# Optimization experiments

Hardware: AMD Instinct MI355X
Metric: run time of the kernel (lower is better)

## Reference

```python
import jax, jax.numpy as jnp
import numpy as np

N = 10000      # num_nodes
E = 320000     # num_edges (before self loops)
F_IN = 256     # num_features
H = 128        # hidden_channels
C = 2          # num_classes
NEG_SLOPE = 0.2  # PyG GATConv default leaky_relu slope


def setup_inputs() -> dict:
    key = jax.random.key(0)
    ks = jax.random.split(key, 12)
    x = jax.random.normal(ks[0], (N, F_IN), dtype=jnp.float32)
    edge_index = jax.random.randint(ks[1], (2, E), 0, N, dtype=jnp.int32)
    s = 0.05
    return {
        "x": x,
        "edge_index": edge_index,
        # GATConv layer 1 (heads=1): lin (no bias), att_src, att_dst, bias
        "W1": jax.random.normal(ks[2], (F_IN, H), dtype=jnp.float32) * s,
        "att_src1": jax.random.normal(ks[3], (H,), dtype=jnp.float32) * s,
        "att_dst1": jax.random.normal(ks[4], (H,), dtype=jnp.float32) * s,
        "b1": jnp.zeros((H,), dtype=jnp.float32),
        # GATConv layer 2
        "W2": jax.random.normal(ks[5], (H, H), dtype=jnp.float32) * s,
        "att_src2": jax.random.normal(ks[6], (H,), dtype=jnp.float32) * s,
        "att_dst2": jax.random.normal(ks[7], (H,), dtype=jnp.float32) * s,
        "b2": jnp.zeros((H,), dtype=jnp.float32),
        # reduce_dim: Linear(H, 1)
        "Wr": jax.random.normal(ks[8], (H, 1), dtype=jnp.float32) * s,
        "br": jnp.zeros((1,), dtype=jnp.float32),
        # classifier: Linear(N, C)
        "Wc": jax.random.normal(ks[9], (N, C), dtype=jnp.float32) * s,
        "bc": jnp.zeros((C,), dtype=jnp.float32),
    }


def _gat_conv(x, src, dst, W, att_src, att_dst, bias):
    """PyG GATConv, heads=1, add_self_loops=True. src/dst include self loops."""
    h = x @ W                           # [N, H]
    a_s = h @ att_src                   # [N]
    a_d = h @ att_dst                   # [N]
    e = a_s[src] + a_d[dst]             # [Etot]
    e = jnp.where(e > 0, e, NEG_SLOPE * e)  # leaky_relu
    # segment softmax over edges grouped by destination node
    m = jax.ops.segment_max(e, dst, num_segments=N)          # [N]
    ex = jnp.exp(e - m[dst])
    z = jax.ops.segment_sum(ex, dst, num_segments=N)         # [N]
    alpha = ex / z[dst]                                       # [Etot]
    out = jax.ops.segment_sum(alpha[:, None] * h[src], dst, num_segments=N)
    return out + bias


def reference(x, edge_index, W1, att_src1, att_dst1, b1,
              W2, att_src2, att_dst2, b2, Wr, br, Wc, bc):
    # add self loops (PyG GATConv default)
    loops = jnp.arange(N, dtype=edge_index.dtype)
    src = jnp.concatenate([edge_index[0], loops])
    dst = jnp.concatenate([edge_index[1], loops])

    h = _gat_conv(x, src, dst, W1, att_src1, att_dst1, b1)
    h = jax.nn.relu(h)
    # dropout(p=0.5) is identity in eval mode
    h = _gat_conv(h, src, dst, W2, att_src2, att_dst2, b2)
    h = jax.nn.relu(h)
    h = h @ Wr + br                     # [N, 1]
    h = h.reshape(1, -1)                # [1, N]
    return h @ Wc + bc                  # [1, C]
```

## Files before the change

kernel.cpp:

```cpp
#include <hip/hip_runtime.h>
#include <hip/hip_bf16.h>

#define NN 10000
#define EE 320000
#define ET (EE + NN)
#define FIN 256
#define HD 128
#define NEG 0.2f



__global__ void k_zero_i(int* __restrict__ p, int n) {
    int i = blockIdx.x * blockDim.x + threadIdx.x;
    if (i < n) p[i] = 0;
}

__global__ void k_hist(const int* __restrict__ ei, int* __restrict__ counts) {
    int i = blockIdx.x * blockDim.x + threadIdx.x;
    if (i >= ET) return;
    int d = (i < EE) ? ei[EE + i] : (i - EE);
    atomicAdd(&counts[d], 1);
}

__global__ void k_scan(const int* __restrict__ counts,
                       int* __restrict__ offsets,
                       int* __restrict__ cursor) {
    const int CHUNK = 40;
    __shared__ int sums[256];
    int t = threadIdx.x;
    int base = t * CHUNK;
    int s = 0;
    for (int i = 0; i < CHUNK; i++) {
        int idx = base + i;
        if (idx < NN) s += counts[idx];
    }
    sums[t] = s;
    __syncthreads();
    for (int off = 1; off < 256; off <<= 1) {
        int v = (t >= off) ? sums[t - off] : 0;
        __syncthreads();
        sums[t] += v;
        __syncthreads();
    }
    int run = (t > 0) ? sums[t - 1] : 0;
    for (int i = 0; i < CHUNK; i++) {
        int idx = base + i;
        if (idx < NN) {
            offsets[idx] = run;
            cursor[idx]  = run;
            run += counts[idx];
        }
    }
    if (t == 255) offsets[NN] = sums[255];
}

__global__ void k_scatter(const int* __restrict__ ei, int* __restrict__ cursor,
                          int* __restrict__ srclist) {
    int i = blockIdx.x * blockDim.x + threadIdx.x;
    if (i >= ET) return;
    int s, d;
    if (i < EE) { s = ei[i]; d = ei[EE + i]; }
    else        { s = i - EE; d = s; }
    int pos = atomicAdd(&cursor[d], 1);
    srclist[pos] = s;
}


__global__ void k_gemm1(const float* __restrict__ x,
                        const float* __restrict__ W,
                        const float* __restrict__ atts,
                        const float* __restrict__ attd,
                        float* __restrict__ h,
                        float* __restrict__ a_s,
                        float* __restrict__ a_d) {
    __shared__ float xs[8 * FIN];
    __shared__ float red[4];
    int t = threadIdx.x;
    int m0 = blockIdx.x * 8;
    const float4* xv = (const float4*)(x + (size_t)m0 * FIN);
    float4* xsv = (float4*)xs;
    #pragma unroll
    for (int i = 0; i < 4; i++)
        xsv[t + 128 * i] = xv[t + 128 * i];
    __syncthreads();

    float acc[8] = {0.f,0.f,0.f,0.f,0.f,0.f,0.f,0.f};
    for (int k = 0; k < FIN; k += 4) {
        float w0 = W[(k + 0) * HD + t];
        float w1 = W[(k + 1) * HD + t];
        float w2 = W[(k + 2) * HD + t];
        float w3 = W[(k + 3) * HD + t];
        #pragma unroll
        for (int m = 0; m < 8; m++) {
            float4 xk = *(const float4*)&xs[m * FIN + k];
            acc[m] += xk.x * w0;
            acc[m] += xk.y * w1;
            acc[m] += xk.z * w2;
            acc[m] += xk.w * w3;
        }
    }

    float at_s = atts[t], at_d = attd[t];
    int lane = t & 63, wid = t >> 6;
    #pragma unroll
    for (int m = 0; m < 8; m++) {
        h[(size_t)(m0 + m) * HD + t] = acc[m];
        float vs = acc[m] * at_s, vd = acc[m] * at_d;
        #pragma unroll
        for (int off = 32; off > 0; off >>= 1) {
            vs += __shfl_down(vs, off);
            vd += __shfl_down(vd, off);
        }
        if (lane == 0) { red[wid] = vs; red[2 + wid] = vd; }
        __syncthreads();
        if (t == 0) {
            a_s[m0 + m] = red[0] + red[1];
            a_d[m0 + m] = red[2] + red[3];
        }
        __syncthreads();
    }
}


__global__ void k_gemm2(const float* __restrict__ x,
                        const float* __restrict__ W,
                        const float* __restrict__ atts,
                        const float* __restrict__ attd,
                        float* __restrict__ h,
                        float* __restrict__ a_s,
                        float* __restrict__ a_d) {
    __shared__ float xs[8 * HD];
    __shared__ float red[4];
    int t = threadIdx.x;
    int m0 = blockIdx.x * 8;
    const float4* xv = (const float4*)(x + (size_t)m0 * HD);
    float4* xsv = (float4*)xs;
    #pragma unroll
    for (int i = 0; i < 2; i++)
        xsv[t + 128 * i] = xv[t + 128 * i];
    __syncthreads();

    float acc[8] = {0.f,0.f,0.f,0.f,0.f,0.f,0.f,0.f};
    for (int k = 0; k < HD; k += 4) {
        float w0 = W[(k + 0) * HD + t];
        float w1 = W[(k + 1) * HD + t];
        float w2 = W[(k + 2) * HD + t];
        float w3 = W[(k + 3) * HD + t];
        #pragma unroll
        for (int m = 0; m < 8; m++) {
            float4 xk = *(const float4*)&xs[m * HD + k];
            acc[m] += xk.x * w0;
            acc[m] += xk.y * w1;
            acc[m] += xk.z * w2;
            acc[m] += xk.w * w3;
        }
    }

    float at_s = atts[t], at_d = attd[t];
    int lane = t & 63, wid = t >> 6;
    #pragma unroll
    for (int m = 0; m < 8; m++) {
        h[(size_t)(m0 + m) * HD + t] = acc[m];
        float vs = acc[m] * at_s, vd = acc[m] * at_d;
        #pragma unroll
        for (int off = 32; off > 0; off >>= 1) {
            vs += __shfl_down(vs, off);
            vd += __shfl_down(vd, off);
        }
        if (lane == 0) { red[wid] = vs; red[2 + wid] = vd; }
        __syncthreads();
        if (t == 0) {
            a_s[m0 + m] = red[0] + red[1];
            a_d[m0 + m] = red[2] + red[3];
        }
        __syncthreads();
    }
}


__device__ __forceinline__ float edge_exp(float as_v, float adn) {
    float e = as_v + adn;
    e = (e > 0.f) ? e : NEG * e;
    return expf(e);
}

__global__ void k_agg1(const int* __restrict__ offsets,
                       const int* __restrict__ srclist,
                       const float* __restrict__ a_s,
                       const float* __restrict__ a_d,
                       const float* __restrict__ h,
                       const float* __restrict__ bias,
                       float* __restrict__ g) {
    int node = blockIdx.x;
    int t = threadIdx.x;
    int beg = offsets[node], end = offsets[node + 1];
    float adn = a_d[node];
    float acc = 0.f, z = 0.f;
    int p = beg;
    for (; p + 4 <= end; p += 4) {
        int s0 = srclist[p], s1 = srclist[p + 1], s2 = srclist[p + 2], s3 = srclist[p + 3];
        float h0 = h[(size_t)s0 * HD + t];
        float h1 = h[(size_t)s1 * HD + t];
        float h2 = h[(size_t)s2 * HD + t];
        float h3 = h[(size_t)s3 * HD + t];
        float x0 = edge_exp(a_s[s0], adn);
        float x1 = edge_exp(a_s[s1], adn);
        float x2 = edge_exp(a_s[s2], adn);
        float x3 = edge_exp(a_s[s3], adn);
        z += x0 + x1 + x2 + x3;
        acc += x0 * h0 + x1 * h1 + x2 * h2 + x3 * h3;
    }
    for (; p < end; p++) {
        int s = srclist[p];
        float hv = h[(size_t)s * HD + t];
        float ex = edge_exp(a_s[s], adn);
        z += ex;
        acc += ex * hv;
    }
    float o = acc / z + bias[t];
    g[(size_t)node * HD + t] = (o > 0.f) ? o : 0.f;
}

__global__ void k_agg2(const int* __restrict__ offsets,
                       const int* __restrict__ srclist,
                       const float* __restrict__ a_s,
                       const float* __restrict__ a_d,
                       const float* __restrict__ h,
                       const float* __restrict__ bias,
                       const float* __restrict__ Wr,
                       const float* __restrict__ br,
                       float* __restrict__ r) {
    __shared__ float red[128];
    int node = blockIdx.x;
    int t = threadIdx.x;
    int beg = offsets[node], end = offsets[node + 1];
    float adn = a_d[node];
    float acc = 0.f, z = 0.f;
    int p = beg;
    for (; p + 4 <= end; p += 4) {
        int s0 = srclist[p], s1 = srclist[p + 1], s2 = srclist[p + 2], s3 = srclist[p + 3];
        float h0 = h[(size_t)s0 * HD + t];
        float h1 = h[(size_t)s1 * HD + t];
        float h2 = h[(size_t)s2 * HD + t];
        float h3 = h[(size_t)s3 * HD + t];
        float x0 = edge_exp(a_s[s0], adn);
        float x1 = edge_exp(a_s[s1], adn);
        float x2 = edge_exp(a_s[s2], adn);
        float x3 = edge_exp(a_s[s3], adn);
        z += x0 + x1 + x2 + x3;
        acc += x0 * h0 + x1 * h1 + x2 * h2 + x3 * h3;
    }
    for (; p < end; p++) {
        int s = srclist[p];
        float hv = h[(size_t)s * HD + t];
        float ex = edge_exp(a_s[s], adn);
        z += ex;
        acc += ex * hv;
    }
    float o = acc / z + bias[t];
    o = (o > 0.f) ? o : 0.f;
    red[t] = o * Wr[t];
    __syncthreads();
    for (int off = 64; off > 0; off >>= 1) {
        if (t < off) red[t] += red[t + off];
        __syncthreads();
    }
    if (t == 0) r[node] = red[0] + br[0];
}


__global__ void k_cls(const float* __restrict__ r,
                      const float* __restrict__ Wc,
                      const float* __restrict__ bc,
                      float* __restrict__ out) {
    __shared__ float r0[256], r1[256];
    int t = threadIdx.x;
    float c0 = 0.f, c1 = 0.f;
    for (int n = t; n < NN; n += 256) {
        float rv = r[n];
        c0 += rv * Wc[2 * n];
        c1 += rv * Wc[2 * n + 1];
    }
    r0[t] = c0; r1[t] = c1;
    __syncthreads();
    for (int off = 128; off > 0; off >>= 1) {
        if (t < off) { r0[t] += r0[t + off]; r1[t] += r1[t + off]; }
        __syncthreads();
    }
    if (t == 0) {
        out[0] = r0[0] + bc[0];
        out[1] = r1[0] + bc[1];
    }
}


extern "C" void kernel_launch(void* const* d_in, const int* in_sizes, int n_in,
                              void* d_out, int out_size, void* d_ws, size_t ws_size,
                              hipStream_t stream) {
    const float* x    = (const float*)d_in[0];
    const int*   ei   = (const int*)d_in[1];
    const float* W1   = (const float*)d_in[2];
    const float* as1  = (const float*)d_in[3];
    const float* ad1  = (const float*)d_in[4];
    const float* b1   = (const float*)d_in[5];
    const float* W2   = (const float*)d_in[6];
    const float* as2  = (const float*)d_in[7];
    const float* ad2  = (const float*)d_in[8];
    const float* b2   = (const float*)d_in[9];
    const float* Wr   = (const float*)d_in[10];
    const float* br   = (const float*)d_in[11];
    const float* Wc   = (const float*)d_in[12];
    const float* bc   = (const float*)d_in[13];
    float* out = (float*)d_out;

    float* h    = (float*)d_ws;
    float* g1   = h + (size_t)NN * HD;
    float* a_s  = g1 + (size_t)NN * HD;
    float* a_d  = a_s + NN;
    float* r    = a_d + NN;
    int* counts  = (int*)(r + NN);
    int* offsets = counts + NN;
    int* cursor  = offsets + NN + 1;
    int* srclist = cursor + NN;

    const int TPB = 256;
    const int gET = (ET + TPB - 1) / TPB;
    const int gNN = (NN + TPB - 1) / TPB;

    k_zero_i<<<gNN, TPB, 0, stream>>>(counts, NN);
    k_hist<<<gET, TPB, 0, stream>>>(ei, counts);
    k_scan<<<1, 256, 0, stream>>>(counts, offsets, cursor);
    k_scatter<<<gET, TPB, 0, stream>>>(ei, cursor, srclist);

    k_gemm1<<<NN / 8, 128, 0, stream>>>(x, W1, as1, ad1, h, a_s, a_d);
    k_agg1<<<NN, 128, 0, stream>>>(offsets, srclist, a_s, a_d, h, b1, g1);

    k_gemm2<<<NN / 8, 128, 0, stream>>>(g1, W2, as2, ad2, h, a_s, a_d);
    k_agg2<<<NN, 128, 0, stream>>>(offsets, srclist, a_s, a_d, h, b2, Wr, br, r);

    k_cls<<<1, 256, 0, stream>>>(r, Wc, bc, out);
}
```

Before: 266.3 us.

## Use wave-per-node aggregation, 16-row GEMM tiles, fast exp and memset

The aggregation kernels now give each node one 64-lane wavefront, with four nodes per 256-thread block. Each lane reads a float2 of the source features, and the reduce_dim dot product is done with wave shuffles instead of a shared-memory tree. The GEMM kernels drop the LDS staging of x, read x rows directly from global memory, and compute 16 rows per block. They also replace the per-row double __syncthreads with a single sync at the end. The zero-init kernel becomes hipMemsetAsync and expf becomes __expf, which reduces accuracy slightly and makes the GEMM rely on cache hits for the broadcast x loads.

```diff
diff --git a/kernel.cpp b/kernel.cpp
--- a/kernel.cpp
+++ b/kernel.cpp
@@ -9,11 +9,6 @@
 #define NEG 0.2f
 
 
-
-__global__ void k_zero_i(int* __restrict__ p, int n) {
-    int i = blockIdx.x * blockDim.x + threadIdx.x;
-    if (i < n) p[i] = 0;
-}
 
 __global__ void k_hist(const int* __restrict__ ei, int* __restrict__ counts) {
     int i = blockIdx.x * blockDim.x + threadIdx.x;
@@ -73,52 +68,42 @@
                         float* __restrict__ h,
                         float* __restrict__ a_s,
                         float* __restrict__ a_d) {
-    __shared__ float xs[8 * FIN];
-    __shared__ float red[4];
     int t = threadIdx.x;
-    int m0 = blockIdx.x * 8;
-    const float4* xv = (const float4*)(x + (size_t)m0 * FIN);
-    float4* xsv = (float4*)xs;
-    #pragma unroll
-    for (int i = 0; i < 4; i++)
-        xsv[t + 128 * i] = xv[t + 128 * i];
-    __syncthreads();
-
-    float acc[8] = {0.f,0.f,0.f,0.f,0.f,0.f,0.f,0.f};
+    int m0 = blockIdx.x * 16;
+    const float* xb = x + (size_t)m0 * FIN;
+    float acc[16];
+    #pragma unroll
+    for (int m = 0; m < 16; m++) acc[m] = 0.f;
+
     for (int k = 0; k < FIN; k += 4) {
         float w0 = W[(k + 0) * HD + t];
         float w1 = W[(k + 1) * HD + t];
         float w2 = W[(k + 2) * HD + t];
         float w3 = W[(k + 3) * HD + t];
         #pragma unroll
-        for (int m = 0; m < 8; m++) {
-            float4 xk = *(const float4*)&xs[m * FIN + k];
-            acc[m] += xk.x * w0;
-            acc[m] += xk.y * w1;
-            acc[m] += xk.z * w2;
-            acc[m] += xk.w * w3;
-        }
-    }
-
-    float at_s = atts[t], at_d = attd[t];
-    int lane = t & 63, wid = t >> 6;
-    #pragma unroll
-    for (int m = 0; m < 8; m++) {
+        for (int m = 0; m < 16; m++) {
+            float4 xk = *(const float4*)(xb + (size_t)m * FIN + k);
+            acc[m] += xk.x * w0 + xk.y * w1 + xk.z * w2 + xk.w * w3;
+        }
+    }
+
+    float ats = atts[t], atd = attd[t];
+    __shared__ float ps[2][2][16];
+    int wv = t >> 6, ln = t & 63;
+    #pragma unroll
+    for (int m = 0; m < 16; m++) {
         h[(size_t)(m0 + m) * HD + t] = acc[m];
-        float vs = acc[m] * at_s, vd = acc[m] * at_d;
+        float vs = acc[m] * ats, vd = acc[m] * atd;
         #pragma unroll
         for (int off = 32; off > 0; off >>= 1) {
             vs += __shfl_down(vs, off);
             vd += __shfl_down(vd, off);
         }
-        if (lane == 0) { red[wid] = vs; red[2 + wid] = vd; }
-        __syncthreads();
-        if (t == 0) {
-            a_s[m0 + m] = red[0] + red[1];
-            a_d[m0 + m] = red[2] + red[3];
-        }
-        __syncthreads();
-    }
+        if (ln == 0) { ps[0][wv][m] = vs; ps[1][wv][m] = vd; }
+    }
+    __syncthreads();
+    if (t < 16) a_s[m0 + t] = ps[0][0][t] + ps[0][1][t];
+    else if (t < 32) a_d[m0 + t - 16] = ps[1][0][t - 16] + ps[1][1][t - 16];
 }
 
 
@@ -129,143 +114,140 @@
                         float* __restrict__ h,
                         float* __restrict__ a_s,
                         float* __restrict__ a_d) {
-    __shared__ float xs[8 * HD];
-    __shared__ float red[4];
     int t = threadIdx.x;
-    int m0 = blockIdx.x * 8;
-    const float4* xv = (const float4*)(x + (size_t)m0 * HD);
-    float4* xsv = (float4*)xs;
-    #pragma unroll
-    for (int i = 0; i < 2; i++)
-        xsv[t + 128 * i] = xv[t + 128 * i];
-    __syncthreads();
-
-    float acc[8] = {0.f,0.f,0.f,0.f,0.f,0.f,0.f,0.f};
+    int m0 = blockIdx.x * 16;
+    const float* xb = x + (size_t)m0 * HD;
+    float acc[16];
+    #pragma unroll
+    for (int m = 0; m < 16; m++) acc[m] = 0.f;
+
     for (int k = 0; k < HD; k += 4) {
         float w0 = W[(k + 0) * HD + t];
         float w1 = W[(k + 1) * HD + t];
         float w2 = W[(k + 2) * HD + t];
         float w3 = W[(k + 3) * HD + t];
         #pragma unroll
-        for (int m = 0; m < 8; m++) {
-            float4 xk = *(const float4*)&xs[m * HD + k];
-            acc[m] += xk.x * w0;
-            acc[m] += xk.y * w1;
-            acc[m] += xk.z * w2;
-            acc[m] += xk.w * w3;
-        }
-    }
-
-    float at_s = atts[t], at_d = attd[t];
-    int lane = t & 63, wid = t >> 6;
-    #pragma unroll
-    for (int m = 0; m < 8; m++) {
+        for (int m = 0; m < 16; m++) {
+            float4 xk = *(const float4*)(xb + (size_t)m * HD + k);
+            acc[m] += xk.x * w0 + xk.y * w1 + xk.z * w2 + xk.w * w3;
+        }
+    }
+
+    float ats = atts[t], atd = attd[t];
+    __shared__ float ps[2][2][16];
+    int wv = t >> 6, ln = t & 63;
+    #pragma unroll
+    for (int m = 0; m < 16; m++) {
         h[(size_t)(m0 + m) * HD + t] = acc[m];
-        float vs = acc[m] * at_s, vd = acc[m] * at_d;
+        float vs = acc[m] * ats, vd = acc[m] * atd;
         #pragma unroll
         for (int off = 32; off > 0; off >>= 1) {
             vs += __shfl_down(vs, off);
             vd += __shfl_down(vd, off);
         }
-        if (lane == 0) { red[wid] = vs; red[2 + wid] = vd; }
-        __syncthreads();
-        if (t == 0) {
-            a_s[m0 + m] = red[0] + red[1];
-            a_d[m0 + m] = red[2] + red[3];
-        }
-        __syncthreads();
-    }
-}
-
-
-__device__ __forceinline__ float edge_exp(float as_v, float adn) {
+        if (ln == 0) { ps[0][wv][m] = vs; ps[1][wv][m] = vd; }
+    }
+    __syncthreads();
+    if (t < 16) a_s[m0 + t] = ps[0][0][t] + ps[0][1][t];
+    else if (t < 32) a_d[m0 + t - 16] = ps[1][0][t - 16] + ps[1][1][t - 16];
+}
+
+
+__device__ __forceinline__ float edge_w(float as_v, float adn) {
     float e = as_v + adn;
     e = (e > 0.f) ? e : NEG * e;
-    return expf(e);
+    return __expf(e);
 }
 
 __global__ void k_agg1(const int* __restrict__ offsets,
                        const int* __restrict__ srclist,
                        const float* __restrict__ a_s,
                        const float* __restrict__ a_d,
-                       const float* __restrict__ h,
+                       const float2* __restrict__ h2,
                        const float* __restrict__ bias,
                        float* __restrict__ g) {
-    int node = blockIdx.x;
-    int t = threadIdx.x;
+    int node = blockIdx.x * 4 + (threadIdx.x >> 6);
+    int l = threadIdx.x & 63;
     int beg = offsets[node], end = offsets[node + 1];
     float adn = a_d[node];
-    float acc = 0.f, z = 0.f;
+    float ax = 0.f, ay = 0.f, z = 0.f;
     int p = beg;
     for (; p + 4 <= end; p += 4) {
         int s0 = srclist[p], s1 = srclist[p + 1], s2 = srclist[p + 2], s3 = srclist[p + 3];
-        float h0 = h[(size_t)s0 * HD + t];
-        float h1 = h[(size_t)s1 * HD + t];
-        float h2 = h[(size_t)s2 * HD + t];
-        float h3 = h[(size_t)s3 * HD + t];
-        float x0 = edge_exp(a_s[s0], adn);
-        float x1 = edge_exp(a_s[s1], adn);
-        float x2 = edge_exp(a_s[s2], adn);
-        float x3 = edge_exp(a_s[s3], adn);
-        z += x0 + x1 + x2 + x3;
-        acc += x0 * h0 + x1 * h1 + x2 * h2 + x3 * h3;
+        float2 h0 = h2[(size_t)s0 * 64 + l];
+        float2 h1 = h2[(size_t)s1 * 64 + l];
+        float2 hv2 = h2[(size_t)s2 * 64 + l];
+        float2 h3 = h2[(size_t)s3 * 64 + l];
+        float w0 = edge_w(a_s[s0], adn);
+        float w1 = edge_w(a_s[s1], adn);
+        float w2 = edge_w(a_s[s2], adn);
+        float w3 = edge_w(a_s[s3], adn);
+        z += (w0 + w1) + (w2 + w3);
+        ax += w0 * h0.x + w1 * h1.x + w2 * hv2.x + w3 * h3.x;
+        ay += w0 * h0.y + w1 * h1.y + w2 * hv2.y + w3 * h3.y;
     }
     for (; p < end; p++) {
         int s = srclist[p];
-        float hv = h[(size_t)s * HD + t];
-        float ex = edge_exp(a_s[s], adn);
-        z += ex;
-        acc += ex * hv;
-    }
-    float o = acc / z + bias[t];
-    g[(size_t)node * HD + t] = (o > 0.f) ? o : 0.f;
+        float2 hv = h2[(size_t)s * 64 + l];
+        float w = edge_w(a_s[s], adn);
+        z += w;
+        ax += w * hv.x;
+        ay += w * hv.y;
+    }
+    float2 b = *(const float2*)&bias[2 * l];
+    float ox = ax / z + b.x, oy = ay / z + b.y;
+    float2 o;
+    o.x = (ox > 0.f) ? ox : 0.f;
+    o.y = (oy > 0.f) ? oy : 0.f;
+    *(float2*)&g[(size_t)node * HD + 2 * l] = o;
 }
 
 __global__ void k_agg2(const int* __restrict__ offsets,
                        const int* __restrict__ srclist,
                        const float* __restrict__ a_s,
                        const float* __restrict__ a_d,
-                       const float* __restrict__ h,
+                       const float2* __restrict__ h2,
                        const float* __restrict__ bias,
                        const float* __restrict__ Wr,
                        const float* __restrict__ br,
                        float* __restrict__ r) {
-    __shared__ float red[128];
-    int node = blockIdx.x;
-    int t = threadIdx.x;
+    int node = blockIdx.x * 4 + (threadIdx.x >> 6);
+    int l = threadIdx.x & 63;
     int beg = offsets[node], end = offsets[node + 1];
     float adn = a_d[node];
-    float acc = 0.f, z = 0.f;
+    float ax = 0.f, ay = 0.f, z = 0.f;
     int p = beg;
     for (; p + 4 <= end; p += 4) {
         int s0 = srclist[p], s1 = srclist[p + 1], s2 = srclist[p + 2], s3 = srclist[p + 3];
-        float h0 = h[(size_t)s0 * HD + t];
-        float h1 = h[(size_t)s1 * HD + t];
-        float h2 = h[(size_t)s2 * HD + t];
-        float h3 = h[(size_t)s3 * HD + t];
-        float x0 = edge_exp(a_s[s0], adn);
-        float x1 = edge_exp(a_s[s1], adn);
-        float x2 = edge_exp(a_s[s2], adn);
-        float x3 = edge_exp(a_s[s3], adn);
-        z += x0 + x1 + x2 + x3;
-        acc += x0 * h0 + x1 * h1 + x2 * h2 + x3 * h3;
+        float2 h0 = h2[(size_t)s0 * 64 + l];
+        float2 h1 = h2[(size_t)s1 * 64 + l];
+        float2 hv2 = h2[(size_t)s2 * 64 + l];
+        float2 h3 = h2[(size_t)s3 * 64 + l];
+        float w0 = edge_w(a_s[s0], adn);
+        float w1 = edge_w(a_s[s1], adn);
+        float w2 = edge_w(a_s[s2], adn);
+        float w3 = edge_w(a_s[s3], adn);
+        z += (w0 + w1) + (w2 + w3);
+        ax += w0 * h0.x + w1 * h1.x + w2 * hv2.x + w3 * h3.x;
+        ay += w0 * h0.y + w1 * h1.y + w2 * hv2.y + w3 * h3.y;
     }
     for (; p < end; p++) {
         int s = srclist[p];
-        float hv = h[(size_t)s * HD + t];
-        float ex = edge_exp(a_s[s], adn);
-        z += ex;
-        acc += ex * hv;
-    }
-    float o = acc / z + bias[t];
-    o = (o > 0.f) ? o : 0.f;
-    red[t] = o * Wr[t];
-    __syncthreads();
-    for (int off = 64; off > 0; off >>= 1) {
-        if (t < off) red[t] += red[t + off];
-        __syncthreads();
-    }
-    if (t == 0) r[node] = red[0] + br[0];
+        float2 hv = h2[(size_t)s * 64 + l];
+        float w = edge_w(a_s[s], adn);
+        z += w;
+        ax += w * hv.x;
+        ay += w * hv.y;
+    }
+    float2 b = *(const float2*)&bias[2 * l];
+    float ox = ax / z + b.x, oy = ay / z + b.y;
+    ox = (ox > 0.f) ? ox : 0.f;
+    oy = (oy > 0.f) ? oy : 0.f;
+    float2 wr = *(const float2*)&Wr[2 * l];
+    float part = ox * wr.x + oy * wr.y;
+    #pragma unroll
+    for (int off = 32; off > 0; off >>= 1) part += __shfl_down(part, off);
+    if (l == 0) r[node] = part + br[0];
 }
 
 
@@ -325,18 +307,17 @@
 
     const int TPB = 256;
     const int gET = (ET + TPB - 1) / TPB;
-    const int gNN = (NN + TPB - 1) / TPB;
-
-    k_zero_i<<<gNN, TPB, 0, stream>>>(counts, NN);
+
+    hipMemsetAsync(counts, 0, NN * sizeof(int), stream);
     k_hist<<<gET, TPB, 0, stream>>>(ei, counts);
     k_scan<<<1, 256, 0, stream>>>(counts, offsets, cursor);
     k_scatter<<<gET, TPB, 0, stream>>>(ei, cursor, srclist);
 
-    k_gemm1<<<NN / 8, 128, 0, stream>>>(x, W1, as1, ad1, h, a_s, a_d);
-    k_agg1<<<NN, 128, 0, stream>>>(offsets, srclist, a_s, a_d, h, b1, g1);
-
-    k_gemm2<<<NN / 8, 128, 0, stream>>>(g1, W2, as2, ad2, h, a_s, a_d);
-    k_agg2<<<NN, 128, 0, stream>>>(offsets, srclist, a_s, a_d, h, b2, Wr, br, r);
+    k_gemm1<<<NN / 16, 128, 0, stream>>>(x, W1, as1, ad1, h, a_s, a_d);
+    k_agg1<<<NN / 4, 256, 0, stream>>>(offsets, srclist, a_s, a_d, (const float2*)h, b1, g1);
+
+    k_gemm2<<<NN / 16, 128, 0, stream>>>(g1, W2, as2, ad2, h, a_s, a_d);
+    k_agg2<<<NN / 4, 256, 0, stream>>>(offsets, srclist, a_s, a_d, (const float2*)h, b2, Wr, br, r);
 
     k_cls<<<1, 256, 0, stream>>>(r, Wc, bc, out);
 }
```

After: 290.3 us. 1.09x slower.
